# Kernel tuning notes

Measured on AMD Instinct MI355X. Metric: run time of the kernel, lower is better.

The kernel has to match this reference:

```python
import jax, jax.numpy as jnp
import numpy as np

NEG_INF = -1.0e9  # matches the torch code's -1000000000.0 fill


def setup_inputs() -> dict:
    key = jax.random.key(0)
    k1, k2, k3, k4 = jax.random.split(key, 4)
    B, Lq, Lk, D = 8, 2048, 2048, 128
    queries = jax.random.normal(k1, (B, Lq, D), dtype=jnp.float32)
    keys = jax.random.normal(k2, (B, Lk, D), dtype=jnp.float32)
    values = jax.random.normal(k3, (B, Lk, D), dtype=jnp.float32)
    valid_length = jax.random.randint(k4, (B,), 1, Lk + 1, dtype=jnp.int32)
    return {"queries": queries, "keys": keys, "values": values,
            "valid_length": valid_length}


def reference(queries, keys, values, valid_length):
    d = queries.shape[-1]
    # scores: [B, Lq, Lk]
    scores = jnp.einsum("bqd,bkd->bqk", queries, keys) / jnp.sqrt(
        jnp.asarray(d, dtype=queries.dtype))
    # per-batch valid key length broadcast over all queries
    Lk = scores.shape[-1]
    mask = jnp.arange(Lk)[None, None, :] >= valid_length[:, None, None]  # [B,1,Lk]
    scores = jnp.where(mask, NEG_INF, scores)
    attn = jax.nn.softmax(scores, axis=-1)
    # dropout p=0.0 -> identity (eval-equivalent)
    return jnp.einsum("bqk,bkd->bqd", attn, values)
```

## Files before the change

kernel.cpp:

```cpp
#include <hip/hip_runtime.h>


#define NB     8
#define LQ     2048
#define LK     2048
#define DH     128
#define KT     32
#define NTILES 64
#define SCL2E  0.12751744f

typedef float f32x4 __attribute__((ext_vector_type(4)));
typedef __bf16 bf16x8 __attribute__((ext_vector_type(8)));
typedef unsigned short u16x4 __attribute__((ext_vector_type(4)));
typedef unsigned short u16x8 __attribute__((ext_vector_type(8)));
typedef unsigned int u32x4 __attribute__((ext_vector_type(4)));

#define KWS_OFF   0ull
#define VWS_OFF   (4ull << 20)
#define WS_NEED   (8ull << 20)

static __device__ __forceinline__ unsigned short f2bf(float f) {
    unsigned int u = __builtin_bit_cast(unsigned int, f);
    u += 0x7FFFu + ((u >> 16) & 1u);
    return (unsigned short)(u >> 16);
}

static __device__ __forceinline__ unsigned int cvtpk(float lo, float hi) {
    unsigned int r;
    asm("v_cvt_pk_bf16_f32 %0, %1, %2" : "=v"(r) : "v"(lo), "v"(hi));
    return r;
}

__global__ __launch_bounds__(256)
void prepass(const float* __restrict__ Kg, const float* __restrict__ Vg,
             const int* __restrict__ VLg,
             unsigned short* __restrict__ Kws, unsigned short* __restrict__ Vws) {
    __shared__ unsigned short Kl[KT][136];
    __shared__ unsigned short Vt[DH][40];
    const int tid = threadIdx.x;
    const int b = blockIdx.x & 7;
    const int t = blockIdx.x >> 3;
    if (t * KT >= VLg[b]) return;
    const size_t gbase = ((size_t)b * LK + (size_t)t * KT) * DH;
    const size_t tbase = (size_t)(b * NTILES + t) * 4096;
    #pragma unroll
    for (int i = 0; i < 4; ++i) {
        int e4 = tid + 256 * i;
        int row = e4 >> 5;
        int c4 = (e4 & 31) * 4;
        float4 kv = *reinterpret_cast<const float4*>(Kg + gbase + (size_t)row * DH + c4);
        u16x4 uk = { f2bf(kv.x), f2bf(kv.y), f2bf(kv.z), f2bf(kv.w) };
        *reinterpret_cast<u16x4*>(&Kl[row][c4]) = uk;
        float4 vv = *reinterpret_cast<const float4*>(Vg + gbase + (size_t)row * DH + c4);
        Vt[c4 + 0][row] = f2bf(vv.x);
        Vt[c4 + 1][row] = f2bf(vv.y);
        Vt[c4 + 2][row] = f2bf(vv.z);
        Vt[c4 + 3][row] = f2bf(vv.w);
    }
    __syncthreads();
    #pragma unroll
    for (int i = 0; i < 2; ++i) {
        int u = tid + 256 * i;
        int sl = u >> 6;
        int l = u & 63;
        int krow = 2 * (l & 15) + (sl & 1);
        int kcol = (sl >> 1) * 32 + (l >> 4) * 8;
        u16x8 kk = *reinterpret_cast<const u16x8*>(&Kl[krow][kcol]);
        *reinterpret_cast<u16x8*>(Kws + tbase + u * 8) = kk;
        int vcol = sl * 16 + (l & 15);
        int k0 = (l >> 4) * 8;
        u16x8 vv8 = *reinterpret_cast<const u16x8*>(&Vt[vcol][k0]);
        *reinterpret_cast<u16x8*>(Vws + tbase + u * 8) = vv8;
    }
}

__global__ __launch_bounds__(256, 2)
void attn_full(const float* __restrict__ Qg, const int* __restrict__ VLg,
               const unsigned short* __restrict__ Kws,
               const unsigned short* __restrict__ Vws,
               float* __restrict__ Og) {
    __shared__ __align__(16) char shbuf[33024];

    const int tid  = threadIdx.x;
    const int lane = tid & 63;
    const int wv   = tid >> 6;
    const int r    = lane & 15;
    const int grp  = lane >> 4;

    unsigned short* Plds = reinterpret_cast<unsigned short*>(shbuf) + wv * 1280;

    const int bid = blockIdx.x;
    const int b  = bid & 7;
    const int qb = bid >> 3;

    const int vl = VLg[b];
    const int nt = (vl + 31) >> 5;
    const bool anymask = (vl & 31) != 0;
    const int q0 = qb * 32;

    bf16x8 qf0[4], qf1[4];
    #pragma unroll
    for (int rb = 0; rb < 2; ++rb) {
        const float* qrow = Qg + ((size_t)(b * LQ + q0 + rb * 16 + r)) * DH + grp * 8;
        #pragma unroll
        for (int c = 0; c < 4; ++c) {
            float4 f0 = *reinterpret_cast<const float4*>(qrow + c * 32);
            float4 f1 = *reinterpret_cast<const float4*>(qrow + c * 32 + 4);
            u32x4 tw;
            tw[0] = cvtpk(f0.x * SCL2E, f0.y * SCL2E);
            tw[1] = cvtpk(f0.z * SCL2E, f0.w * SCL2E);
            tw[2] = cvtpk(f1.x * SCL2E, f1.y * SCL2E);
            tw[3] = cvtpk(f1.z * SCL2E, f1.w * SCL2E);
            if (rb == 0) qf0[c] = __builtin_bit_cast(bf16x8, tw);
            else         qf1[c] = __builtin_bit_cast(bf16x8, tw);
        }
    }

    const f32x4 zero4 = {0.f, 0.f, 0.f, 0.f};
    f32x4 acc[2][8];
    #pragma unroll
    for (int rb = 0; rb < 2; ++rb)
        #pragma unroll
        for (int d8 = 0; d8 < 8; ++d8) acc[rb][d8] = zero4;
    float lsum[2][4] = {{0.f, 0.f, 0.f, 0.f}, {0.f, 0.f, 0.f, 0.f}};

    const unsigned short* kp = Kws + (size_t)(b * NTILES + wv) * 4096 + lane * 8;
    const unsigned short* vp = Vws + (size_t)(b * NTILES + wv) * 4096 + lane * 8;

    bf16x8 kreg[8], vreg[8];
    if (wv < nt) {
        #pragma unroll
        for (int sl = 0; sl < 8; ++sl) {
            kreg[sl] = *reinterpret_cast<const bf16x8*>(kp + sl * 512);
            vreg[sl] = *reinterpret_cast<const bf16x8*>(vp + sl * 512);
        }
    }

    for (int t = wv; t < nt; t += 4) {
        const bool lastt = (t == nt - 1);
        f32x4 s00 = zero4, s01 = zero4, s10 = zero4, s11 = zero4;
        #pragma unroll
        for (int c = 0; c < 4; ++c) {
            s00 = __builtin_amdgcn_mfma_f32_16x16x32_bf16(qf0[c], kreg[2 * c],     s00, 0, 0, 0);
            s01 = __builtin_amdgcn_mfma_f32_16x16x32_bf16(qf0[c], kreg[2 * c + 1], s01, 0, 0, 0);
            s10 = __builtin_amdgcn_mfma_f32_16x16x32_bf16(qf1[c], kreg[2 * c],     s10, 0, 0, 0);
            s11 = __builtin_amdgcn_mfma_f32_16x16x32_bf16(qf1[c], kreg[2 * c + 1], s11, 0, 0, 0);
        }
        if (t + 4 < nt) {
            kp += 4 * 4096;
            #pragma unroll
            for (int sl = 0; sl < 8; ++sl)
                kreg[sl] = *reinterpret_cast<const bf16x8*>(kp + sl * 512);
        }

        const int kk = t * KT + 2 * r;
        const bool mm = lastt & anymask;
        const bool m0 = mm && (kk >= vl);
        const bool m1 = mm && (kk + 1 >= vl);
        #pragma unroll
        for (int j = 0; j < 4; ++j) {
            float a0 = m0 ? -1e9f : s00[j];
            float a1 = m1 ? -1e9f : s01[j];
            float b0 = m0 ? -1e9f : s10[j];
            float b1 = m1 ? -1e9f : s11[j];
            float p00 = exp2f(a0), p01 = exp2f(a1);
            float p10 = exp2f(b0), p11 = exp2f(b1);
            lsum[0][j] += p00 + p01;
            lsum[1][j] += p10 + p11;
            *reinterpret_cast<unsigned int*>(&Plds[(grp * 4 + j) * 40 + 2 * r]) =
                cvtpk(p00, p01);
            *reinterpret_cast<unsigned int*>(&Plds[640 + (grp * 4 + j) * 40 + 2 * r]) =
                cvtpk(p10, p11);
        }
        bf16x8 pa0 = *reinterpret_cast<const bf16x8*>(&Plds[r * 40 + grp * 8]);
        bf16x8 pa1 = *reinterpret_cast<const bf16x8*>(&Plds[640 + r * 40 + grp * 8]);

        #pragma unroll
        for (int d8 = 0; d8 < 8; ++d8) {
            acc[0][d8] = __builtin_amdgcn_mfma_f32_16x16x32_bf16(pa0, vreg[d8], acc[0][d8], 0, 0, 0);
            acc[1][d8] = __builtin_amdgcn_mfma_f32_16x16x32_bf16(pa1, vreg[d8], acc[1][d8], 0, 0, 0);
        }
        if (t + 4 < nt) {
            vp += 4 * 4096;
            #pragma unroll
            for (int sl = 0; sl < 8; ++sl)
                vreg[sl] = *reinterpret_cast<const bf16x8*>(vp + sl * 512);
        }
    }

    #pragma unroll
    for (int rb = 0; rb < 2; ++rb) {
        #pragma unroll
        for (int j = 0; j < 4; ++j) {
            float v = lsum[rb][j];
            #pragma unroll
            for (int d = 1; d < 16; d <<= 1) v += __shfl_xor(v, d);
            lsum[rb][j] = v;
        }
    }

    float* A  = reinterpret_cast<float*>(shbuf);
    float* Bz = reinterpret_cast<float*>(shbuf + 16384);
    float* Ls = reinterpret_cast<float*>(shbuf + 32768);
    __syncthreads();
    if (wv == 1 || wv == 3) {
        float* R = (wv == 1) ? A : Bz;
        #pragma unroll
        for (int rb = 0; rb < 2; ++rb)
            #pragma unroll
            for (int d8 = 0; d8 < 8; ++d8) {
                int ps = ((rb * 8 + d8) + lane) & 15;
                *reinterpret_cast<f32x4*>(&R[lane * 64 + ps * 4]) = acc[rb][d8];
            }
    }
    if (wv != 0 && r == 0) {
        #pragma unroll
        for (int rb = 0; rb < 2; ++rb)
            #pragma unroll
            for (int j = 0; j < 4; ++j)
                Ls[(wv - 1) * 32 + rb * 16 + grp * 4 + j] = lsum[rb][j];
    }
    __syncthreads();
    if (wv == 0 || wv == 2) {
        const float* R = (wv == 0) ? A : Bz;
        #pragma unroll
        for (int rb = 0; rb < 2; ++rb)
            #pragma unroll
            for (int d8 = 0; d8 < 8; ++d8) {
                int ps = ((rb * 8 + d8) + lane) & 15;
                acc[rb][d8] += *reinterpret_cast<const f32x4*>(&R[lane * 64 + ps * 4]);
            }
    }
    __syncthreads();
    if (wv == 2) {
        #pragma unroll
        for (int rb = 0; rb < 2; ++rb)
            #pragma unroll
            for (int d8 = 0; d8 < 8; ++d8) {
                int ps = ((rb * 8 + d8) + lane) & 15;
                *reinterpret_cast<f32x4*>(&A[lane * 64 + ps * 4]) = acc[rb][d8];
            }
    }
    __syncthreads();
    if (wv != 0) return;

    #pragma unroll
    for (int rb = 0; rb < 2; ++rb) {
        #pragma unroll
        for (int d8 = 0; d8 < 8; ++d8) {
            int ps = ((rb * 8 + d8) + lane) & 15;
            acc[rb][d8] += *reinterpret_cast<const f32x4*>(&A[lane * 64 + ps * 4]);
        }
        #pragma unroll
        for (int j = 0; j < 4; ++j)
            lsum[rb][j] += Ls[rb * 16 + grp * 4 + j] + Ls[32 + rb * 16 + grp * 4 + j]
                         + Ls[64 + rb * 16 + grp * 4 + j];
    }

    #pragma unroll
    for (int rb = 0; rb < 2; ++rb)
        #pragma unroll
        for (int d8 = 0; d8 < 8; ++d8)
            #pragma unroll
            for (int j = 0; j < 4; ++j)
                Og[((size_t)(b * LQ + q0 + rb * 16 + grp * 4 + j)) * 128 + d8 * 16 + r] =
                    acc[rb][d8][j] / lsum[rb][j];
}

#define SCALE 0.08838834764831845f
__global__ __launch_bounds__(256)
void attn_fwd(const float* __restrict__ Qg, const float* __restrict__ Kg,
              const float* __restrict__ Vg, const int* __restrict__ VLg,
              float* __restrict__ Og) {
    __shared__ unsigned short Klds[KT][DH];
    __shared__ unsigned short Vt[DH][KT];
    __shared__ unsigned short Pl[4][16][KT];
    const int tid = threadIdx.x;
    const int lane = tid & 63;
    const int wv = tid >> 6;
    const int r = lane & 15;
    const int grp = lane >> 4;
    const int qblocks = LQ / 64;
    const int b = blockIdx.x / qblocks;
    const int qb = blockIdx.x % qblocks;
    const int q0 = qb * 64 + wv * 16;
    const int vl = VLg[b];
    const int ntiles = (vl + KT - 1) / KT;
    bf16x8 qf[4];
    {
        const float* qrow = Qg + ((size_t)(b * LQ + q0 + r)) * DH + grp * 8;
        #pragma unroll
        for (int c = 0; c < 4; ++c) {
            float4 f0 = *reinterpret_cast<const float4*>(qrow + c * 32);
            float4 f1 = *reinterpret_cast<const float4*>(qrow + c * 32 + 4);
            u16x8 t;
            t[0] = f2bf(f0.x); t[1] = f2bf(f0.y); t[2] = f2bf(f0.z); t[3] = f2bf(f0.w);
            t[4] = f2bf(f1.x); t[5] = f2bf(f1.y); t[6] = f2bf(f1.z); t[7] = f2bf(f1.w);
            qf[c] = __builtin_bit_cast(bf16x8, t);
        }
    }
    const f32x4 zero4 = {0.f, 0.f, 0.f, 0.f};
    f32x4 acc[8];
    #pragma unroll
    for (int d8 = 0; d8 < 8; ++d8) acc[d8] = zero4;
    float mrun[4] = {-1e30f, -1e30f, -1e30f, -1e30f};
    float lsum[4] = {0.f, 0.f, 0.f, 0.f};
    for (int t = 0; t < ntiles; ++t) {
        const int kb = t * KT;
        __syncthreads();
        {
            const size_t kvbase = ((size_t)b * LK + kb) * DH;
            #pragma unroll
            for (int i = 0; i < 4; ++i) {
                int e4 = tid + 256 * i;
                int row = e4 >> 5;
                int c4 = (e4 & 31) * 4;
                float4 kv = *reinterpret_cast<const float4*>(Kg + kvbase + (size_t)row * DH + c4);
                u16x4 uk = { f2bf(kv.x), f2bf(kv.y), f2bf(kv.z), f2bf(kv.w) };
                *reinterpret_cast<u16x4*>(&Klds[row][c4]) = uk;
                float4 vv = *reinterpret_cast<const float4*>(Vg + kvbase + (size_t)row * DH + c4);
                Vt[c4 + 0][row] = f2bf(vv.x);
                Vt[c4 + 1][row] = f2bf(vv.y);
                Vt[c4 + 2][row] = f2bf(vv.z);
                Vt[c4 + 3][row] = f2bf(vv.w);
            }
        }
        __syncthreads();
        f32x4 s0 = zero4, s1 = zero4;
        #pragma unroll
        for (int c = 0; c < 4; ++c) {
            bf16x8 k0 = *reinterpret_cast<const bf16x8*>(&Klds[r][c * 32 + grp * 8]);
            bf16x8 k1 = *reinterpret_cast<const bf16x8*>(&Klds[16 + r][c * 32 + grp * 8]);
            s0 = __builtin_amdgcn_mfma_f32_16x16x32_bf16(qf[c], k0, s0, 0, 0, 0);
            s1 = __builtin_amdgcn_mfma_f32_16x16x32_bf16(qf[c], k1, s1, 0, 0, 0);
        }
        const bool msk0 = (kb + r) >= vl;
        const bool msk1 = (kb + 16 + r) >= vl;
        float alpha[4];
        #pragma unroll
        for (int j = 0; j < 4; ++j) {
            float v0 = msk0 ? -1e9f : s0[j] * SCALE;
            float v1 = msk1 ? -1e9f : s1[j] * SCALE;
            float mx = fmaxf(v0, v1);
            #pragma unroll
            for (int d = 1; d < 16; d <<= 1) mx = fmaxf(mx, __shfl_xor(mx, d));
            float mnew = fmaxf(mrun[j], mx);
            float a = __expf(mrun[j] - mnew);
            float p0 = __expf(v0 - mnew);
            float p1 = __expf(v1 - mnew);
            float rs = p0 + p1;
            #pragma unroll
            for (int d = 1; d < 16; d <<= 1) rs += __shfl_xor(rs, d);
            lsum[j] = lsum[j] * a + rs;
            mrun[j] = mnew;
            alpha[j] = a;
            Pl[wv][grp * 4 + j][r] = f2bf(p0);
            Pl[wv][grp * 4 + j][16 + r] = f2bf(p1);
        }
        #pragma unroll
        for (int d8 = 0; d8 < 8; ++d8) {
            #pragma unroll
            for (int j = 0; j < 4; ++j) acc[d8][j] *= alpha[j];
        }
        bf16x8 pa = *reinterpret_cast<const bf16x8*>(&Pl[wv][r][grp * 8]);
        #pragma unroll
        for (int d8 = 0; d8 < 8; ++d8) {
            bf16x8 vf = *reinterpret_cast<const bf16x8*>(&Vt[d8 * 16 + r][grp * 8]);
            acc[d8] = __builtin_amdgcn_mfma_f32_16x16x32_bf16(pa, vf, acc[d8], 0, 0, 0);
        }
    }
    #pragma unroll
    for (int d8 = 0; d8 < 8; ++d8) {
        #pragma unroll
        for (int j = 0; j < 4; ++j) {
            int qr = q0 + grp * 4 + j;
            Og[((size_t)b * LQ + qr) * DH + d8 * 16 + r] = acc[d8][j] / lsum[j];
        }
    }
}

extern "C" void kernel_launch(void* const* d_in, const int* in_sizes, int n_in,
                              void* d_out, int out_size, void* d_ws, size_t ws_size,
                              hipStream_t stream) {
    const float* Q  = (const float*)d_in[0];
    const float* K  = (const float*)d_in[1];
    const float* V  = (const float*)d_in[2];
    const int*   VL = (const int*)d_in[3];
    float* O = (float*)d_out;

    if (ws_size < WS_NEED) {
        dim3 grid(NB * (LQ / 64));
        attn_fwd<<<grid, 256, 0, stream>>>(Q, K, V, VL, O);
        return;
    }
    unsigned short* Kws = (unsigned short*)((char*)d_ws + KWS_OFF);
    unsigned short* Vws = (unsigned short*)((char*)d_ws + VWS_OFF);

    prepass<<<dim3(NB * NTILES), 256, 0, stream>>>(K, V, VL, Kws, Vws);
    attn_full<<<dim3(NB * 64), 256, 0, stream>>>(Q, VL, Kws, Vws, O);
}
```

Measured before the change: 37.14 us.

## Halve query rows per block to double grid size and raise occupancy

Each attn_full block now handles 16 query rows instead of 32, so the grid doubles to 1024 blocks and per-wave accumulators, LDS for P and the reduction buffers shrink by half. Launch bounds are raised to 3 blocks per CU. The aim is more parallelism and occupancy on a GPU with many CUs, since 512 blocks left the device underfilled. The cost is that every K/V tile is loaded from the workspace twice as often, and MFMA reuse of each loaded K/V fragment is halved.

After: 45.28 us. 1.22x slower.

```diff
diff --git a/kernel.cpp b/kernel.cpp
--- a/kernel.cpp
+++ b/kernel.cpp
@@ -74,12 +74,12 @@
     }
 }
 
-__global__ __launch_bounds__(256, 2)
+__global__ __launch_bounds__(256, 3)
 void attn_full(const float* __restrict__ Qg, const int* __restrict__ VLg,
                const unsigned short* __restrict__ Kws,
                const unsigned short* __restrict__ Vws,
                float* __restrict__ Og) {
-    __shared__ __align__(16) char shbuf[33024];
+    __shared__ __align__(16) char shbuf[16768];
 
     const int tid  = threadIdx.x;
     const int lane = tid & 63;
@@ -87,7 +87,7 @@
     const int r    = lane & 15;
     const int grp  = lane >> 4;
 
-    unsigned short* Plds = reinterpret_cast<unsigned short*>(shbuf) + wv * 1280;
+    unsigned short* Plds = reinterpret_cast<unsigned short*>(shbuf) + wv * 640;
 
     const int bid = blockIdx.x;
     const int b  = bid & 7;
@@ -96,12 +96,11 @@
     const int vl = VLg[b];
     const int nt = (vl + 31) >> 5;
     const bool anymask = (vl & 31) != 0;
-    const int q0 = qb * 32;
-
-    bf16x8 qf0[4], qf1[4];
-    #pragma unroll
-    for (int rb = 0; rb < 2; ++rb) {
-        const float* qrow = Qg + ((size_t)(b * LQ + q0 + rb * 16 + r)) * DH + grp * 8;
+    const int q0 = qb * 16;
+
+    bf16x8 qf[4];
+    {
+        const float* qrow = Qg + ((size_t)(b * LQ + q0 + r)) * DH + grp * 8;
         #pragma unroll
         for (int c = 0; c < 4; ++c) {
             float4 f0 = *reinterpret_cast<const float4*>(qrow + c * 32);
@@ -111,18 +110,15 @@
             tw[1] = cvtpk(f0.z * SCL2E, f0.w * SCL2E);
             tw[2] = cvtpk(f1.x * SCL2E, f1.y * SCL2E);
             tw[3] = cvtpk(f1.z * SCL2E, f1.w * SCL2E);
-            if (rb == 0) qf0[c] = __builtin_bit_cast(bf16x8, tw);
-            else         qf1[c] = __builtin_bit_cast(bf16x8, tw);
+            qf[c] = __builtin_bit_cast(bf16x8, tw);
         }
     }
 
     const f32x4 zero4 = {0.f, 0.f, 0.f, 0.f};
-    f32x4 acc[2][8];
-    #pragma unroll
-    for (int rb = 0; rb < 2; ++rb)
-        #pragma unroll
-        for (int d8 = 0; d8 < 8; ++d8) acc[rb][d8] = zero4;
-    float lsum[2][4] = {{0.f, 0.f, 0.f, 0.f}, {0.f, 0.f, 0.f, 0.f}};
+    f32x4 acc[8];
+    #pragma unroll
+    for (int d8 = 0; d8 < 8; ++d8) acc[d8] = zero4;
+    float lsum[4] = {0.f, 0.f, 0.f, 0.f};
 
     const unsigned short* kp = Kws + (size_t)(b * NTILES + wv) * 4096 + lane * 8;
     const unsigned short* vp = Vws + (size_t)(b * NTILES + wv) * 4096 + lane * 8;
@@ -138,13 +134,11 @@
 
     for (int t = wv; t < nt; t += 4) {
         const bool lastt = (t == nt - 1);
-        f32x4 s00 = zero4, s01 = zero4, s10 = zero4, s11 = zero4;
+        f32x4 s0 = zero4, s1 = zero4;
         #pragma unroll
         for (int c = 0; c < 4; ++c) {
-            s00 = __builtin_amdgcn_mfma_f32_16x16x32_bf16(qf0[c], kreg[2 * c],     s00, 0, 0, 0);
-            s01 = __builtin_amdgcn_mfma_f32_16x16x32_bf16(qf0[c], kreg[2 * c + 1], s01, 0, 0, 0);
-            s10 = __builtin_amdgcn_mfma_f32_16x16x32_bf16(qf1[c], kreg[2 * c],     s10, 0, 0, 0);
-            s11 = __builtin_amdgcn_mfma_f32_16x16x32_bf16(qf1[c], kreg[2 * c + 1], s11, 0, 0, 0);
+            s0 = __builtin_amdgcn_mfma_f32_16x16x32_bf16(qf[c], kreg[2 * c],     s0, 0, 0, 0);
+            s1 = __builtin_amdgcn_mfma_f32_16x16x32_bf16(qf[c], kreg[2 * c + 1], s1, 0, 0, 0);
         }
         if (t + 4 < nt) {
             kp += 4 * 4096;
@@ -159,27 +153,18 @@
         const bool m1 = mm && (kk + 1 >= vl);
         #pragma unroll
         for (int j = 0; j < 4; ++j) {
-            float a0 = m0 ? -1e9f : s00[j];
-            float a1 = m1 ? -1e9f : s01[j];
-            float b0 = m0 ? -1e9f : s10[j];
-            float b1 = m1 ? -1e9f : s11[j];
-            float p00 = exp2f(a0), p01 = exp2f(a1);
-            float p10 = exp2f(b0), p11 = exp2f(b1);
-            lsum[0][j] += p00 + p01;
-            lsum[1][j] += p10 + p11;
+            float a0 = m0 ? -1e9f : s0[j];
+            float a1 = m1 ? -1e9f : s1[j];
+            float p0 = exp2f(a0), p1 = exp2f(a1);
+            lsum[j] += p0 + p1;
             *reinterpret_cast<unsigned int*>(&Plds[(grp * 4 + j) * 40 + 2 * r]) =
-                cvtpk(p00, p01);
-            *reinterpret_cast<unsigned int*>(&Plds[640 + (grp * 4 + j) * 40 + 2 * r]) =
-                cvtpk(p10, p11);
-        }
-        bf16x8 pa0 = *reinterpret_cast<const bf16x8*>(&Plds[r * 40 + grp * 8]);
-        bf16x8 pa1 = *reinterpret_cast<const bf16x8*>(&Plds[640 + r * 40 + grp * 8]);
-
-        #pragma unroll
-        for (int d8 = 0; d8 < 8; ++d8) {
-            acc[0][d8] = __builtin_amdgcn_mfma_f32_16x16x32_bf16(pa0, vreg[d8], acc[0][d8], 0, 0, 0);
-            acc[1][d8] = __builtin_amdgcn_mfma_f32_16x16x32_bf16(pa1, vreg[d8], acc[1][d8], 0, 0, 0);
-        }
+                cvtpk(p0, p1);
+        }
+        bf16x8 pa = *reinterpret_cast<const bf16x8*>(&Plds[r * 40 + grp * 8]);
+
+        #pragma unroll
+        for (int d8 = 0; d8 < 8; ++d8)
+            acc[d8] = __builtin_amdgcn_mfma_f32_16x16x32_bf16(pa, vreg[d8], acc[d8], 0, 0, 0);
         if (t + 4 < nt) {
             vp += 4 * 4096;
             #pragma unroll
@@ -189,82 +174,65 @@
     }
 
     #pragma unroll
-    for (int rb = 0; rb < 2; ++rb) {
-        #pragma unroll
-        for (int j = 0; j < 4; ++j) {
-            float v = lsum[rb][j];
-            #pragma unroll
-            for (int d = 1; d < 16; d <<= 1) v += __shfl_xor(v, d);
-            lsum[rb][j] = v;
-        }
+    for (int j = 0; j < 4; ++j) {
+        float v = lsum[j];
+        #pragma unroll
+        for (int d = 1; d < 16; d <<= 1) v += __shfl_xor(v, d);
+        lsum[j] = v;
     }
 
     float* A  = reinterpret_cast<float*>(shbuf);
-    float* Bz = reinterpret_cast<float*>(shbuf + 16384);
-    float* Ls = reinterpret_cast<float*>(shbuf + 32768);
+    float* Bz = reinterpret_cast<float*>(shbuf + 8192);
+    float* Ls = reinterpret_cast<float*>(shbuf + 16384);
     __syncthreads();
     if (wv == 1 || wv == 3) {
         float* R = (wv == 1) ? A : Bz;
         #pragma unroll
-        for (int rb = 0; rb < 2; ++rb)
-            #pragma unroll
-            for (int d8 = 0; d8 < 8; ++d8) {
-                int ps = ((rb * 8 + d8) + lane) & 15;
-                *reinterpret_cast<f32x4*>(&R[lane * 64 + ps * 4]) = acc[rb][d8];
-            }
+        for (int d8 = 0; d8 < 8; ++d8) {
+            int ps = (d8 + lane) & 7;
+            *reinterpret_cast<f32x4*>(&R[lane * 32 + ps * 4]) = acc[d8];
+        }
     }
     if (wv != 0 && r == 0) {
         #pragma unroll
-        for (int rb = 0; rb < 2; ++rb)
-            #pragma unroll
-            for (int j = 0; j < 4; ++j)
-                Ls[(wv - 1) * 32 + rb * 16 + grp * 4 + j] = lsum[rb][j];
+        for (int j = 0; j < 4; ++j)
+            Ls[(wv - 1) * 16 + grp * 4 + j] = lsum[j];
     }
     __syncthreads();
     if (wv == 0 || wv == 2) {
         const float* R = (wv == 0) ? A : Bz;
         #pragma unroll
-        for (int rb = 0; rb < 2; ++rb)
-            #pragma unroll
-            for (int d8 = 0; d8 < 8; ++d8) {
-                int ps = ((rb * 8 + d8) + lane) & 15;
-                acc[rb][d8] += *reinterpret_cast<const f32x4*>(&R[lane * 64 + ps * 4]);
-            }
+        for (int d8 = 0; d8 < 8; ++d8) {
+            int ps = (d8 + lane) & 7;
+            acc[d8] += *reinterpret_cast<const f32x4*>(&R[lane * 32 + ps * 4]);
+        }
     }
     __syncthreads();
     if (wv == 2) {
         #pragma unroll
-        for (int rb = 0; rb < 2; ++rb)
-            #pragma unroll
-            for (int d8 = 0; d8 < 8; ++d8) {
-                int ps = ((rb * 8 + d8) + lane) & 15;
-                *reinterpret_cast<f32x4*>(&A[lane * 64 + ps * 4]) = acc[rb][d8];
-            }
+        for (int d8 = 0; d8 < 8; ++d8) {
+            int ps = (d8 + lane) & 7;
+            *reinterpret_cast<f32x4*>(&A[lane * 32 + ps * 4]) = acc[d8];
+        }
     }
     __syncthreads();
     if (wv != 0) return;
 
     #pragma unroll
-    for (int rb = 0; rb < 2; ++rb) {
-        #pragma unroll
-        for (int d8 = 0; d8 < 8; ++d8) {
-            int ps = ((rb * 8 + d8) + lane) & 15;
-            acc[rb][d8] += *reinterpret_cast<const f32x4*>(&A[lane * 64 + ps * 4]);
-        }
+    for (int d8 = 0; d8 < 8; ++d8) {
+        int ps = (d8 + lane) & 7;
+        acc[d8] += *reinterpret_cast<const f32x4*>(&A[lane * 32 + ps * 4]);
+    }
+    #pragma unroll
+    for (int j = 0; j < 4; ++j)
+        lsum[j] += Ls[grp * 4 + j] + Ls[16 + grp * 4 + j] + Ls[32 + grp * 4 + j];
+
+    #pragma unroll
+    for (int d8 = 0; d8 < 8; ++d8)
         #pragma unroll
         for (int j = 0; j < 4; ++j)
-            lsum[rb][j] += Ls[rb * 16 + grp * 4 + j] + Ls[32 + rb * 16 + grp * 4 + j]
-                         + Ls[64 + rb * 16 + grp * 4 + j];
-    }
-
-    #pragma unroll
-    for (int rb = 0; rb < 2; ++rb)
-        #pragma unroll
-        for (int d8 = 0; d8 < 8; ++d8)
-            #pragma unroll
-            for (int j = 0; j < 4; ++j)
-                Og[((size_t)(b * LQ + q0 + rb * 16 + grp * 4 + j)) * 128 + d8 * 16 + r] =
-                    acc[rb][d8][j] / lsum[rb][j];
+            Og[((size_t)(b * LQ + q0 + grp * 4 + j)) * 128 + d8 * 16 + r] =
+                acc[d8][j] / lsum[j];
 }
 
 #define SCALE 0.08838834764831845f
@@ -397,5 +365,5 @@
     unsigned short* Vws = (unsigned short*)((char*)d_ws + VWS_OFF);
 
     prepass<<<dim3(NB * NTILES), 256, 0, stream>>>(K, V, VL, Kws, Vws);
-    attn_full<<<dim3(NB * 64), 256, 0, stream>>>(Q, VL, Kws, Vws, O);
-}
+    attn_full<<<dim3(NB * 128), 256, 0, stream>>>(Q, VL, Kws, Vws, O);
+}
```

## Fuse K/V bf16 conversion into attention kernel, drop prepass and workspace

Applied to the files above, without the earlier changes.

Removes the separate prepass kernel that converted K and V to bf16 into a pre-swizzled workspace layout. The attention kernel now reads fp32 K and V straight from global memory and converts to bf16 in registers into the MFMA operand layout. This saves a kernel launch and the workspace write/read round trip. In exchange, each of the 64 query blocks per batch re-reads and re-converts fp32 K/V, doubling bytes per load. The V load becomes strided scalar gathers (8 rows per column), which may be poorly coalesced.

Measured after the change: 79.30 us. 2.14x slower.

```diff
diff --git a/kernel.cpp b/kernel.cpp
--- a/kernel.cpp
+++ b/kernel.cpp
@@ -6,24 +6,11 @@
 #define LK     2048
 #define DH     128
 #define KT     32
-#define NTILES 64
 #define SCL2E  0.12751744f
 
 typedef float f32x4 __attribute__((ext_vector_type(4)));
 typedef __bf16 bf16x8 __attribute__((ext_vector_type(8)));
-typedef unsigned short u16x4 __attribute__((ext_vector_type(4)));
-typedef unsigned short u16x8 __attribute__((ext_vector_type(8)));
 typedef unsigned int u32x4 __attribute__((ext_vector_type(4)));
-
-#define KWS_OFF   0ull
-#define VWS_OFF   (4ull << 20)
-#define WS_NEED   (8ull << 20)
-
-static __device__ __forceinline__ unsigned short f2bf(float f) {
-    unsigned int u = __builtin_bit_cast(unsigned int, f);
-    u += 0x7FFFu + ((u >> 16) & 1u);
-    return (unsigned short)(u >> 16);
-}
 
 static __device__ __forceinline__ unsigned int cvtpk(float lo, float hi) {
     unsigned int r;
@@ -31,53 +18,9 @@
     return r;
 }
 
-__global__ __launch_bounds__(256)
-void prepass(const float* __restrict__ Kg, const float* __restrict__ Vg,
-             const int* __restrict__ VLg,
-             unsigned short* __restrict__ Kws, unsigned short* __restrict__ Vws) {
-    __shared__ unsigned short Kl[KT][136];
-    __shared__ unsigned short Vt[DH][40];
-    const int tid = threadIdx.x;
-    const int b = blockIdx.x & 7;
-    const int t = blockIdx.x >> 3;
-    if (t * KT >= VLg[b]) return;
-    const size_t gbase = ((size_t)b * LK + (size_t)t * KT) * DH;
-    const size_t tbase = (size_t)(b * NTILES + t) * 4096;
-    #pragma unroll
-    for (int i = 0; i < 4; ++i) {
-        int e4 = tid + 256 * i;
-        int row = e4 >> 5;
-        int c4 = (e4 & 31) * 4;
-        float4 kv = *reinterpret_cast<const float4*>(Kg + gbase + (size_t)row * DH + c4);
-        u16x4 uk = { f2bf(kv.x), f2bf(kv.y), f2bf(kv.z), f2bf(kv.w) };
-        *reinterpret_cast<u16x4*>(&Kl[row][c4]) = uk;
-        float4 vv = *reinterpret_cast<const float4*>(Vg + gbase + (size_t)row * DH + c4);
-        Vt[c4 + 0][row] = f2bf(vv.x);
-        Vt[c4 + 1][row] = f2bf(vv.y);
-        Vt[c4 + 2][row] = f2bf(vv.z);
-        Vt[c4 + 3][row] = f2bf(vv.w);
-    }
-    __syncthreads();
-    #pragma unroll
-    for (int i = 0; i < 2; ++i) {
-        int u = tid + 256 * i;
-        int sl = u >> 6;
-        int l = u & 63;
-        int krow = 2 * (l & 15) + (sl & 1);
-        int kcol = (sl >> 1) * 32 + (l >> 4) * 8;
-        u16x8 kk = *reinterpret_cast<const u16x8*>(&Kl[krow][kcol]);
-        *reinterpret_cast<u16x8*>(Kws + tbase + u * 8) = kk;
-        int vcol = sl * 16 + (l & 15);
-        int k0 = (l >> 4) * 8;
-        u16x8 vv8 = *reinterpret_cast<const u16x8*>(&Vt[vcol][k0]);
-        *reinterpret_cast<u16x8*>(Vws + tbase + u * 8) = vv8;
-    }
-}
-
 __global__ __launch_bounds__(256, 2)
-void attn_full(const float* __restrict__ Qg, const int* __restrict__ VLg,
-               const unsigned short* __restrict__ Kws,
-               const unsigned short* __restrict__ Vws,
+void attn_full(const float* __restrict__ Qg, const float* __restrict__ Kg,
+               const float* __restrict__ Vg, const int* __restrict__ VLg,
                float* __restrict__ Og) {
     __shared__ __align__(16) char shbuf[33024];
 
@@ -97,6 +40,9 @@
     const int nt = (vl + 31) >> 5;
     const bool anymask = (vl & 31) != 0;
     const int q0 = qb * 32;
+
+    const float* Kbase = Kg + (size_t)b * LK * DH;
+    const float* Vbase = Vg + (size_t)b * LK * DH;
 
     bf16x8 qf0[4], qf1[4];
     #pragma unroll
@@ -124,16 +70,45 @@
         for (int d8 = 0; d8 < 8; ++d8) acc[rb][d8] = zero4;
     float lsum[2][4] = {{0.f, 0.f, 0.f, 0.f}, {0.f, 0.f, 0.f, 0.f}};
 
-    const unsigned short* kp = Kws + (size_t)(b * NTILES + wv) * 4096 + lane * 8;
-    const unsigned short* vp = Vws + (size_t)(b * NTILES + wv) * 4096 + lane * 8;
-
     bf16x8 kreg[8], vreg[8];
+
+#define LOADK(TT)                                                              \
+    {                                                                          \
+        const float* kp_ = Kbase + ((size_t)(TT) * KT + 2 * r) * DH + grp * 8; \
+        _Pragma("unroll")                                                      \
+        for (int c = 0; c < 4; ++c) {                                          \
+            _Pragma("unroll")                                                  \
+            for (int h = 0; h < 2; ++h) {                                      \
+                const float* p_ = kp_ + (size_t)h * DH + c * 32;               \
+                float4 f0 = *reinterpret_cast<const float4*>(p_);              \
+                float4 f1 = *reinterpret_cast<const float4*>(p_ + 4);          \
+                u32x4 tw;                                                      \
+                tw[0] = cvtpk(f0.x, f0.y); tw[1] = cvtpk(f0.z, f0.w);          \
+                tw[2] = cvtpk(f1.x, f1.y); tw[3] = cvtpk(f1.z, f1.w);          \
+                kreg[c * 2 + h] = __builtin_bit_cast(bf16x8, tw);              \
+            }                                                                  \
+        }                                                                      \
+    }
+
+#define LOADV(TT)                                                              \
+    {                                                                          \
+        const float* vp_ = Vbase + ((size_t)(TT) * KT + grp * 8) * DH + r;     \
+        _Pragma("unroll")                                                      \
+        for (int d8 = 0; d8 < 8; ++d8) {                                       \
+            float tv[8];                                                       \
+            _Pragma("unroll")                                                  \
+            for (int w = 0; w < 8; ++w)                                        \
+                tv[w] = vp_[(size_t)w * DH + d8 * 16];                         \
+            u32x4 tw;                                                          \
+            tw[0] = cvtpk(tv[0], tv[1]); tw[1] = cvtpk(tv[2], tv[3]);          \
+            tw[2] = cvtpk(tv[4], tv[5]); tw[3] = cvtpk(tv[6], tv[7]);          \
+            vreg[d8] = __builtin_bit_cast(bf16x8, tw);                         \
+        }                                                                      \
+    }
+
     if (wv < nt) {
-        #pragma unroll
-        for (int sl = 0; sl < 8; ++sl) {
-            kreg[sl] = *reinterpret_cast<const bf16x8*>(kp + sl * 512);
-            vreg[sl] = *reinterpret_cast<const bf16x8*>(vp + sl * 512);
-        }
+        LOADK(wv)
+        LOADV(wv)
     }
 
     for (int t = wv; t < nt; t += 4) {
@@ -146,12 +121,7 @@
             s10 = __builtin_amdgcn_mfma_f32_16x16x32_bf16(qf1[c], kreg[2 * c],     s10, 0, 0, 0);
             s11 = __builtin_amdgcn_mfma_f32_16x16x32_bf16(qf1[c], kreg[2 * c + 1], s11, 0, 0, 0);
         }
-        if (t + 4 < nt) {
-            kp += 4 * 4096;
-            #pragma unroll
-            for (int sl = 0; sl < 8; ++sl)
-                kreg[sl] = *reinterpret_cast<const bf16x8*>(kp + sl * 512);
-        }
+        if (t + 4 < nt) LOADK(t + 4)
 
         const int kk = t * KT + 2 * r;
         const bool mm = lastt & anymask;
@@ -180,13 +150,10 @@
             acc[0][d8] = __builtin_amdgcn_mfma_f32_16x16x32_bf16(pa0, vreg[d8], acc[0][d8], 0, 0, 0);
             acc[1][d8] = __builtin_amdgcn_mfma_f32_16x16x32_bf16(pa1, vreg[d8], acc[1][d8], 0, 0, 0);
         }
-        if (t + 4 < nt) {
-            vp += 4 * 4096;
-            #pragma unroll
-            for (int sl = 0; sl < 8; ++sl)
-                vreg[sl] = *reinterpret_cast<const bf16x8*>(vp + sl * 512);
-        }
-    }
+        if (t + 4 < nt) LOADV(t + 4)
+    }
+#undef LOADK
+#undef LOADV
 
     #pragma unroll
     for (int rb = 0; rb < 2; ++rb) {
@@ -265,118 +232,6 @@
             for (int j = 0; j < 4; ++j)
                 Og[((size_t)(b * LQ + q0 + rb * 16 + grp * 4 + j)) * 128 + d8 * 16 + r] =
                     acc[rb][d8][j] / lsum[rb][j];
-}
-
-#define SCALE 0.08838834764831845f
-__global__ __launch_bounds__(256)
-void attn_fwd(const float* __restrict__ Qg, const float* __restrict__ Kg,
-              const float* __restrict__ Vg, const int* __restrict__ VLg,
-              float* __restrict__ Og) {
-    __shared__ unsigned short Klds[KT][DH];
-    __shared__ unsigned short Vt[DH][KT];
-    __shared__ unsigned short Pl[4][16][KT];
-    const int tid = threadIdx.x;
-    const int lane = tid & 63;
-    const int wv = tid >> 6;
-    const int r = lane & 15;
-    const int grp = lane >> 4;
-    const int qblocks = LQ / 64;
-    const int b = blockIdx.x / qblocks;
-    const int qb = blockIdx.x % qblocks;
-    const int q0 = qb * 64 + wv * 16;
-    const int vl = VLg[b];
-    const int ntiles = (vl + KT - 1) / KT;
-    bf16x8 qf[4];
-    {
-        const float* qrow = Qg + ((size_t)(b * LQ + q0 + r)) * DH + grp * 8;
-        #pragma unroll
-        for (int c = 0; c < 4; ++c) {
-            float4 f0 = *reinterpret_cast<const float4*>(qrow + c * 32);
-            float4 f1 = *reinterpret_cast<const float4*>(qrow + c * 32 + 4);
-            u16x8 t;
-            t[0] = f2bf(f0.x); t[1] = f2bf(f0.y); t[2] = f2bf(f0.z); t[3] = f2bf(f0.w);
-            t[4] = f2bf(f1.x); t[5] = f2bf(f1.y); t[6] = f2bf(f1.z); t[7] = f2bf(f1.w);
-            qf[c] = __builtin_bit_cast(bf16x8, t);
-        }
-    }
-    const f32x4 zero4 = {0.f, 0.f, 0.f, 0.f};
-    f32x4 acc[8];
-    #pragma unroll
-    for (int d8 = 0; d8 < 8; ++d8) acc[d8] = zero4;
-    float mrun[4] = {-1e30f, -1e30f, -1e30f, -1e30f};
-    float lsum[4] = {0.f, 0.f, 0.f, 0.f};
-    for (int t = 0; t < ntiles; ++t) {
-        const int kb = t * KT;
-        __syncthreads();
-        {
-            const size_t kvbase = ((size_t)b * LK + kb) * DH;
-            #pragma unroll
-            for (int i = 0; i < 4; ++i) {
-                int e4 = tid + 256 * i;
-                int row = e4 >> 5;
-                int c4 = (e4 & 31) * 4;
-                float4 kv = *reinterpret_cast<const float4*>(Kg + kvbase + (size_t)row * DH + c4);
-                u16x4 uk = { f2bf(kv.x), f2bf(kv.y), f2bf(kv.z), f2bf(kv.w) };
-                *reinterpret_cast<u16x4*>(&Klds[row][c4]) = uk;
-                float4 vv = *reinterpret_cast<const float4*>(Vg + kvbase + (size_t)row * DH + c4);
-                Vt[c4 + 0][row] = f2bf(vv.x);
-                Vt[c4 + 1][row] = f2bf(vv.y);
-                Vt[c4 + 2][row] = f2bf(vv.z);
-                Vt[c4 + 3][row] = f2bf(vv.w);
-            }
-        }
-        __syncthreads();
-        f32x4 s0 = zero4, s1 = zero4;
-        #pragma unroll
-        for (int c = 0; c < 4; ++c) {
-            bf16x8 k0 = *reinterpret_cast<const bf16x8*>(&Klds[r][c * 32 + grp * 8]);
-            bf16x8 k1 = *reinterpret_cast<const bf16x8*>(&Klds[16 + r][c * 32 + grp * 8]);
-            s0 = __builtin_amdgcn_mfma_f32_16x16x32_bf16(qf[c], k0, s0, 0, 0, 0);
-            s1 = __builtin_amdgcn_mfma_f32_16x16x32_bf16(qf[c], k1, s1, 0, 0, 0);
-        }
-        const bool msk0 = (kb + r) >= vl;
-        const bool msk1 = (kb + 16 + r) >= vl;
-        float alpha[4];
-        #pragma unroll
-        for (int j = 0; j < 4; ++j) {
-            float v0 = msk0 ? -1e9f : s0[j] * SCALE;
-            float v1 = msk1 ? -1e9f : s1[j] * SCALE;
-            float mx = fmaxf(v0, v1);
-            #pragma unroll
-            for (int d = 1; d < 16; d <<= 1) mx = fmaxf(mx, __shfl_xor(mx, d));
-            float mnew = fmaxf(mrun[j], mx);
-            float a = __expf(mrun[j] - mnew);
-            float p0 = __expf(v0 - mnew);
-            float p1 = __expf(v1 - mnew);
-            float rs = p0 + p1;
-            #pragma unroll
-            for (int d = 1; d < 16; d <<= 1) rs += __shfl_xor(rs, d);
-            lsum[j] = lsum[j] * a + rs;
-            mrun[j] = mnew;
-            alpha[j] = a;
-            Pl[wv][grp * 4 + j][r] = f2bf(p0);
-            Pl[wv][grp * 4 + j][16 + r] = f2bf(p1);
-        }
-        #pragma unroll
-        for (int d8 = 0; d8 < 8; ++d8) {
-            #pragma unroll
-            for (int j = 0; j < 4; ++j) acc[d8][j] *= alpha[j];
-        }
-        bf16x8 pa = *reinterpret_cast<const bf16x8*>(&Pl[wv][r][grp * 8]);
-        #pragma unroll
-        for (int d8 = 0; d8 < 8; ++d8) {
-            bf16x8 vf = *reinterpret_cast<const bf16x8*>(&Vt[d8 * 16 + r][grp * 8]);
-            acc[d8] = __builtin_amdgcn_mfma_f32_16x16x32_bf16(pa, vf, acc[d8], 0, 0, 0);
-        }
-    }
-    #pragma unroll
-    for (int d8 = 0; d8 < 8; ++d8) {
-        #pragma unroll
-        for (int j = 0; j < 4; ++j) {
-            int qr = q0 + grp * 4 + j;
-            Og[((size_t)b * LQ + qr) * DH + d8 * 16 + r] = acc[d8][j] / lsum[j];
-        }
-    }
 }
 
 extern "C" void kernel_launch(void* const* d_in, const int* in_sizes, int n_in,
@@ -388,14 +243,5 @@
     const int*   VL = (const int*)d_in[3];
     float* O = (float*)d_out;
 
-    if (ws_size < WS_NEED) {
-        dim3 grid(NB * (LQ / 64));
-        attn_fwd<<<grid, 256, 0, stream>>>(Q, K, V, VL, O);
-        return;
-    }
-    unsigned short* Kws = (unsigned short*)((char*)d_ws + KWS_OFF);
-    unsigned short* Vws = (unsigned short*)((char*)d_ws + VWS_OFF);
-
-    prepass<<<dim3(NB * NTILES), 256, 0, stream>>>(K, V, VL, Kws, Vws);
-    attn_full<<<dim3(NB * 64), 256, 0, stream>>>(Q, VL, Kws, Vws, O);
+    attn_full<<<dim3(NB * 64), 256, 0, stream>>>(Q, K, V, VL, O);
 }
```

## Stage K tiles through double-buffered LDS via direct global-to-LDS loads

Applied to the files above, without the earlier changes.

K tiles are now prefetched with global_load_lds into a per-wave double buffer in shared memory instead of into registers. Each iteration reads the current tile from LDS and issues the next tile's async load. The intent is to cut VGPR pressure and overlap K fetches with compute. In exchange, shared memory grows to about 74 KB per block, which may limit the two-blocks-per-CU occupancy. A full vmcnt(0) wait each iteration also stalls on the outstanding V register loads.

Measured after the change: 39.77 us. 7.1% more time.

```diff
diff --git a/kernel.cpp b/kernel.cpp
--- a/kernel.cpp
+++ b/kernel.cpp
@@ -29,6 +29,13 @@
     unsigned int r;
     asm("v_cvt_pk_bf16_f32 %0, %1, %2" : "=v"(r) : "v"(lo), "v"(hi));
     return r;
+}
+
+#define AS1 __attribute__((address_space(1)))
+#define AS3 __attribute__((address_space(3)))
+static __device__ __forceinline__ void gload_lds16(const void* g, void* l) {
+    __builtin_amdgcn_global_load_lds((const AS1 unsigned int*)g,
+                                     (AS3 unsigned int*)l, 16, 0, 0);
 }
 
 __global__ __launch_bounds__(256)
@@ -79,7 +86,7 @@
                const unsigned short* __restrict__ Kws,
                const unsigned short* __restrict__ Vws,
                float* __restrict__ Og) {
-    __shared__ __align__(16) char shbuf[33024];
+    __shared__ __align__(16) char shbuf[75776];
 
     const int tid  = threadIdx.x;
     const int lane = tid & 63;
@@ -87,7 +94,8 @@
     const int r    = lane & 15;
     const int grp  = lane >> 4;
 
-    unsigned short* Plds = reinterpret_cast<unsigned short*>(shbuf) + wv * 1280;
+    unsigned short* Plds = reinterpret_cast<unsigned short*>(shbuf + 65536) + wv * 1280;
+    char* kst_base = shbuf + wv * 16384;
 
     const int bid = blockIdx.x;
     const int b  = bid & 7;
@@ -124,39 +132,50 @@
         for (int d8 = 0; d8 < 8; ++d8) acc[rb][d8] = zero4;
     float lsum[2][4] = {{0.f, 0.f, 0.f, 0.f}, {0.f, 0.f, 0.f, 0.f}};
 
-    const unsigned short* kp = Kws + (size_t)(b * NTILES + wv) * 4096 + lane * 8;
+    auto kstage = [&](int buf, int t) {
+        const char* gk = (const char*)(Kws + (size_t)(b * NTILES + t) * 4096);
+        char* lb = kst_base + buf * 8192;
+        #pragma unroll
+        for (int sl = 0; sl < 8; ++sl)
+            gload_lds16(gk + sl * 1024 + lane * 16, lb + sl * 1024);
+    };
+
     const unsigned short* vp = Vws + (size_t)(b * NTILES + wv) * 4096 + lane * 8;
-
-    bf16x8 kreg[8], vreg[8];
+    bf16x8 vreg[8];
     if (wv < nt) {
-        #pragma unroll
-        for (int sl = 0; sl < 8; ++sl) {
-            kreg[sl] = *reinterpret_cast<const bf16x8*>(kp + sl * 512);
+        kstage(0, wv);
+        #pragma unroll
+        for (int sl = 0; sl < 8; ++sl)
             vreg[sl] = *reinterpret_cast<const bf16x8*>(vp + sl * 512);
-        }
-    }
+    }
+    int cur = 0;
 
     for (int t = wv; t < nt; t += 4) {
         const bool lastt = (t == nt - 1);
+        asm volatile("s_waitcnt vmcnt(0)" ::: "memory");
+
+        const unsigned short* Kst =
+            reinterpret_cast<const unsigned short*>(kst_base + cur * 8192);
+        bf16x8 kk[8];
+        #pragma unroll
+        for (int sl = 0; sl < 8; ++sl)
+            kk[sl] = *reinterpret_cast<const bf16x8*>(&Kst[sl * 512 + lane * 8]);
+
+        if (t + 4 < nt) kstage(cur ^ 1, t + 4);
+
         f32x4 s00 = zero4, s01 = zero4, s10 = zero4, s11 = zero4;
         #pragma unroll
         for (int c = 0; c < 4; ++c) {
-            s00 = __builtin_amdgcn_mfma_f32_16x16x32_bf16(qf0[c], kreg[2 * c],     s00, 0, 0, 0);
-            s01 = __builtin_amdgcn_mfma_f32_16x16x32_bf16(qf0[c], kreg[2 * c + 1], s01, 0, 0, 0);
-            s10 = __builtin_amdgcn_mfma_f32_16x16x32_bf16(qf1[c], kreg[2 * c],     s10, 0, 0, 0);
-            s11 = __builtin_amdgcn_mfma_f32_16x16x32_bf16(qf1[c], kreg[2 * c + 1], s11, 0, 0, 0);
-        }
-        if (t + 4 < nt) {
-            kp += 4 * 4096;
-            #pragma unroll
-            for (int sl = 0; sl < 8; ++sl)
-                kreg[sl] = *reinterpret_cast<const bf16x8*>(kp + sl * 512);
-        }
-
-        const int kk = t * KT + 2 * r;
+            s00 = __builtin_amdgcn_mfma_f32_16x16x32_bf16(qf0[c], kk[2 * c],     s00, 0, 0, 0);
+            s01 = __builtin_amdgcn_mfma_f32_16x16x32_bf16(qf0[c], kk[2 * c + 1], s01, 0, 0, 0);
+            s10 = __builtin_amdgcn_mfma_f32_16x16x32_bf16(qf1[c], kk[2 * c],     s10, 0, 0, 0);
+            s11 = __builtin_amdgcn_mfma_f32_16x16x32_bf16(qf1[c], kk[2 * c + 1], s11, 0, 0, 0);
+        }
+
+        const int kkidx = t * KT + 2 * r;
         const bool mm = lastt & anymask;
-        const bool m0 = mm && (kk >= vl);
-        const bool m1 = mm && (kk + 1 >= vl);
+        const bool m0 = mm && (kkidx >= vl);
+        const bool m1 = mm && (kkidx + 1 >= vl);
         #pragma unroll
         for (int j = 0; j < 4; ++j) {
             float a0 = m0 ? -1e9f : s00[j];
@@ -186,6 +205,7 @@
             for (int sl = 0; sl < 8; ++sl)
                 vreg[sl] = *reinterpret_cast<const bf16x8*>(vp + sl * 512);
         }
+        cur ^= 1;
     }
 
     #pragma unroll
```
